# Performance work log

Measured on AMD Instinct MI355X. Metric: run time of the kernel, lower is better.

The kernel has to match this reference:

```python
import jax, jax.numpy as jnp
import numpy as np

N = 100000   # nodes
E = 1000000  # edges (avg degree 10)
F_IN, H1, H2, C = 128, 64, 64, 16


def setup_inputs() -> dict:
    key = jax.random.key(0)
    ks = jax.random.split(key, 10)
    x = jax.random.normal(ks[0], (N, F_IN), dtype=jnp.float32)
    edge_src = jax.random.randint(ks[1], (E,), 0, N, dtype=jnp.int32)
    edge_dst = jax.random.randint(ks[2], (E,), 0, N, dtype=jnp.int32)
    # normalized-adjacency-like positive edge weights (~1/deg scale)
    edge_val = jax.random.uniform(ks[3], (E,), dtype=jnp.float32) * 0.1
    def glorot(k, fan_in, fan_out):
        s = np.float32(1.0 / np.sqrt(fan_in))
        return jax.random.normal(k, (fan_in, fan_out), dtype=jnp.float32) * s
    W1 = glorot(ks[4], F_IN, H1)
    W2 = glorot(ks[5], H1, H2)
    W3 = glorot(ks[6], H2, C)
    b1 = jnp.zeros((H1,), jnp.float32)
    b2 = jnp.zeros((H2,), jnp.float32)
    b3 = jnp.zeros((C,), jnp.float32)
    return {"x": x, "edge_val": edge_val, "W1": W1, "b1": b1,
            "W2": W2, "b2": b2, "W3": W3, "b3": b3,
            "edge_src": edge_src, "edge_dst": edge_dst}


def gcn_layer(h, W, b, edge_src, edge_dst, edge_val):
    # support = h @ W ; out = spmm(adj, support) + b
    support = h @ W                                  # [N, d_out]
    msg = support[edge_src] * edge_val[:, None]      # [E, d_out] gather + scale
    agg = jax.ops.segment_sum(msg, edge_dst, num_segments=N)  # scatter-add
    return agg + b


def reference(x, edge_val, W1, b1, W2, b2, W3, b3, edge_src, edge_dst):
    # eval mode: F.dropout(training=False) is identity
    h = jax.nn.relu(gcn_layer(x, W1, b1, edge_src, edge_dst, edge_val))
    h = jax.nn.relu(gcn_layer(h, W2, b2, edge_src, edge_dst, edge_val))
    return gcn_layer(h, W3, b3, edge_src, edge_dst, edge_val)  # [N, C] logits
```

## Files before the change

kernel.cpp:

```cpp
#include <hip/hip_runtime.h>
#include <stdint.h>

#define N_NODES 100000
#define N_EDGES 1000000
#define NBUCK 98

typedef __attribute__((ext_vector_type(8))) __bf16 bf16x8;
typedef __attribute__((ext_vector_type(4))) float f32x4;

static __device__ __forceinline__ float bf2f(unsigned short u) {
    return __uint_as_float(((unsigned int)u) << 16);
}
static __device__ __forceinline__ unsigned short f2bf(float f) {
    unsigned int u = __float_as_uint(f);
    unsigned int r = (u + 0x7FFFu + ((u >> 16) & 1u)) >> 16;
    return (unsigned short)r;
}
static __device__ __forceinline__ float4 ld4_half(const unsigned short* p) {
    ushort4 u = *(const ushort4*)p;
    return make_float4(bf2f(u.x), bf2f(u.y), bf2f(u.z), bf2f(u.w));
}
static __device__ __forceinline__ void st4_half(unsigned short* p, float4 f) {
    ushort4 u;
    u.x = f2bf(f.x); u.y = f2bf(f.y); u.z = f2bf(f.z); u.w = f2bf(f.w);
    *(ushort4*)p = u;
}

static __device__ __forceinline__ float ldf(const void* p, size_t i, int bf) {
    return bf ? bf2f(((const unsigned short*)p)[i]) : ((const float*)p)[i];
}
static __device__ __forceinline__ float4 ldf4(const void* p, size_t i, int bf) {
    if (bf) return ld4_half((const unsigned short*)p + i);
    return *(const float4*)((const float*)p + i);
}

__global__ __launch_bounds__(256) void detect_kernel(const unsigned short* __restrict__ xs,
                                                     int* __restrict__ flag) {
    __shared__ int sz;
    if (threadIdx.x == 0) sz = 0;
    __syncthreads();
    int z = 0;
    for (int i = threadIdx.x; i < 1024; i += 256) {
        float av = fabsf(bf2f(xs[2 * i]));
        if (!(av <= 1048576.0f) || (av != 0.0f && av < 9.5367431640625e-07f)) z++;
    }
    atomicAdd(&sz, z);
    __syncthreads();
    if (threadIdx.x == 0) *flag = (sz > 256) ? 0 : 1;
}

__global__ __launch_bounds__(256) void bhist_kernel(const int* __restrict__ dst,
                                                    int* __restrict__ bcount) {
    __shared__ int cnt[NBUCK];
    int tid = threadIdx.x;
    for (int i = tid; i < NBUCK; i += 256) cnt[i] = 0;
    __syncthreads();
    int e0 = blockIdx.x * 4096;
#pragma unroll
    for (int i = 0; i < 16; ++i) {
        int e = e0 + i * 256 + tid;
        if (e < N_EDGES) atomicAdd(&cnt[dst[e] >> 10], 1);
    }
    __syncthreads();
    for (int i = tid; i < NBUCK; i += 256) {
        int c = cnt[i];
        if (c) atomicAdd(&bcount[i], c);
    }
}

__global__ __launch_bounds__(128) void bscan_kernel(const int* __restrict__ bcount,
                                                    int* __restrict__ bstart,
                                                    int* __restrict__ bcursor) {
    __shared__ int sh[128];
    int tid = threadIdx.x;
    int v = (tid < NBUCK) ? bcount[tid] : 0;
    sh[tid] = v;
    __syncthreads();
    for (int off = 1; off < 128; off <<= 1) {
        int t = 0;
        if (tid >= off) t = sh[tid - off];
        __syncthreads();
        if (tid >= off) sh[tid] += t;
        __syncthreads();
    }
    if (tid < NBUCK) {
        int excl = sh[tid] - v;
        bstart[tid] = excl;
        bcursor[tid] = excl;
    }
    if (tid == NBUCK - 1) bstart[NBUCK] = sh[tid];
}

__global__ __launch_bounds__(256) void part_kernel(const int* __restrict__ src,
                                                   const int* __restrict__ dst,
                                                   const void* __restrict__ val,
                                                   int* __restrict__ bcursor,
                                                   int2* __restrict__ part,
                                                   const int* __restrict__ flagp) {
    __shared__ int cnt[NBUCK];
    __shared__ int base[NBUCK];
    const int bf = *flagp;
    const int tid = threadIdx.x;
    const int e0 = blockIdx.x * 2048;
    for (int i = tid; i < NBUCK; i += 256) cnt[i] = 0;
    __syncthreads();
    int rank[8], bkt[8], pk[8], vb[8];
#pragma unroll
    for (int i = 0; i < 8; ++i) {
        int e = e0 + i * 256 + tid;
        bkt[i] = -1;
        if (e < N_EDGES) {
            int d = dst[e];
            int b = d >> 10;
            bkt[i] = b;
            pk[i] = src[e] | ((d & 1023) << 17);
            vb[i] = __float_as_int(ldf(val, e, bf));
            rank[i] = atomicAdd(&cnt[b], 1);
        }
    }
    __syncthreads();
    for (int i = tid; i < NBUCK; i += 256) {
        int c = cnt[i];
        base[i] = c ? atomicAdd(&bcursor[i], c) : 0;
    }
    __syncthreads();
#pragma unroll
    for (int i = 0; i < 8; ++i) {
        if (bkt[i] >= 0) part[(size_t)base[bkt[i]] + rank[i]] = make_int2(pk[i], vb[i]);
    }
}

__global__ __launch_bounds__(512) void place_kernel(const int* __restrict__ bstart,
                                                    const int2* __restrict__ part,
                                                    int* __restrict__ row_start,
                                                    int2* __restrict__ csr_rec) {
    __shared__ int cnt[1024];
    __shared__ int sums[512];
    const int tid = threadIdx.x;
    const int b = blockIdx.x;
    const int row0 = b << 10;
    const int nrows = min(1024, N_NODES - row0);
    const int s = bstart[b], e = bstart[b + 1];

    for (int i = tid; i < 1024; i += 512) cnt[i] = 0;
    __syncthreads();
    for (int j = s + tid; j < e; j += 512) {
        unsigned p = (unsigned)part[j].x;
        atomicAdd(&cnt[p >> 17], 1);
    }
    __syncthreads();
    int a0 = cnt[2 * tid], a1 = cnt[2 * tid + 1];
    int ts = a0 + a1;
    sums[tid] = ts;
    __syncthreads();
    for (int off = 1; off < 512; off <<= 1) {
        int t = 0;
        if (tid >= off) t = sums[tid - off];
        __syncthreads();
        if (tid >= off) sums[tid] += t;
        __syncthreads();
    }
    int excl = sums[tid] - ts;
    cnt[2 * tid] = s + excl;
    cnt[2 * tid + 1] = s + excl + a0;
    if (2 * tid < nrows)     row_start[row0 + 2 * tid] = s + excl;
    if (2 * tid + 1 < nrows) row_start[row0 + 2 * tid + 1] = s + excl + a0;
    if (b == NBUCK - 1 && tid == 0) row_start[N_NODES] = e;
    __syncthreads();
    for (int j = s + tid; j < e; j += 512) {
        int2 r = part[j];
        unsigned p = (unsigned)r.x;
        int pos = atomicAdd(&cnt[p >> 17], 1);
        csr_rec[pos] = make_int2((int)(p & 0x1FFFFu), r.y);
    }
}

template <int M>
static __device__ __forceinline__ void quad_gather(const unsigned short* __restrict__ supc,
                                                   const int2* __restrict__ csr_rec,
                                                   int s, int b1, int b2, int b3, int e,
                                                   float4 acc[4]) {
    if (s >= e) return;
    int2 r[8];
#pragma unroll
    for (int t = 0; t < 8; ++t) r[t] = csr_rec[min(s + t, e - 1)];
    for (int j = s; j < e; j += 8) {
        float4 sp[8];
#pragma unroll
        for (int t = 0; t < 8; ++t) sp[t] = ld4_half(supc + (size_t)r[t].x * M);
        float wv[8];
#pragma unroll
        for (int t = 0; t < 8; ++t) wv[t] = (j + t < e) ? __int_as_float(r[t].y) : 0.0f;
        int jn = j + 8;
        if (jn < e) {
#pragma unroll
            for (int t = 0; t < 8; ++t) r[t] = csr_rec[min(jn + t, e - 1)];
        }
#pragma unroll
        for (int t = 0; t < 8; ++t) {
            int idx = j + t;
            float c0 = (idx < b1) ? wv[t] : 0.0f;
            float c1 = (idx < b2) ? wv[t] : 0.0f;
            float c2 = (idx < b3) ? wv[t] : 0.0f;
            float w0 = c0;
            float w1 = c1 - c0;
            float w2 = c2 - c1;
            float w3 = wv[t] - c2;
            acc[0].x += w0 * sp[t].x; acc[0].y += w0 * sp[t].y; acc[0].z += w0 * sp[t].z; acc[0].w += w0 * sp[t].w;
            acc[1].x += w1 * sp[t].x; acc[1].y += w1 * sp[t].y; acc[1].z += w1 * sp[t].z; acc[1].w += w1 * sp[t].w;
            acc[2].x += w2 * sp[t].x; acc[2].y += w2 * sp[t].y; acc[2].z += w2 * sp[t].z; acc[2].w += w2 * sp[t].w;
            acc[3].x += w3 * sp[t].x; acc[3].y += w3 * sp[t].y; acc[3].z += w3 * sp[t].z; acc[3].w += w3 * sp[t].w;
        }
    }
}

template <int K, int M, bool DYNIN>
__global__ __launch_bounds__(256, 4) void mgemm_kernel(const void* __restrict__ hv_,
                                                       const void* __restrict__ W,
                                                       unsigned short* __restrict__ out,
                                                       const int* __restrict__ flagp) {
    constexpr int KP = K + 8;
    constexpr int NC = M / 16;
    constexpr int NK = K / 32;
    constexpr int NT = (N_NODES + 63) / 64;

    __shared__ unsigned short wt[M][KP];

    const int bf = *flagp;
    const int tid = threadIdx.x;

    for (int i = tid; i < K * M; i += 256) {
        int k = i / M, m = i % M;
        wt[m][k] = f2bf(ldf(W, i, bf));
    }
    __syncthreads();

    const int lane = tid & 63;
    const int qd = lane >> 4;
    const int ln = lane & 15;
    const int wrow = (tid >> 6) * 16;

    for (int tile = blockIdx.x; tile < NT; tile += gridDim.x) {
        const int row = tile * 64 + wrow + ln;
        const bool ok = row < N_NODES;

        f32x4 acc[NC];
#pragma unroll
        for (int c = 0; c < NC; ++c) acc[c] = (f32x4){0.f, 0.f, 0.f, 0.f};

#pragma unroll
        for (int ks = 0; ks < NK; ++ks) {
            bf16x8 a;
            if (ok) {
                const size_t base = (size_t)row * K + ks * 32 + qd * 8;
                if (DYNIN && !bf) {
                    const float* xp = (const float*)hv_ + base;
                    float4 f0 = *(const float4*)xp;
                    float4 f1 = *(const float4*)(xp + 4);
                    ushort4 uu[2];
                    uu[0].x = f2bf(f0.x); uu[0].y = f2bf(f0.y); uu[0].z = f2bf(f0.z); uu[0].w = f2bf(f0.w);
                    uu[1].x = f2bf(f1.x); uu[1].y = f2bf(f1.y); uu[1].z = f2bf(f1.z); uu[1].w = f2bf(f1.w);
                    a = *(const bf16x8*)uu;
                } else {
                    a = *(const bf16x8*)((const unsigned short*)hv_ + base);
                }
            } else {
                a = (bf16x8)(__bf16)0.0f;
            }
#pragma unroll
            for (int c = 0; c < NC; ++c) {
                bf16x8 b = *(const bf16x8*)&wt[c * 16 + ln][ks * 32 + qd * 8];
                acc[c] = __builtin_amdgcn_mfma_f32_16x16x32_bf16(a, b, acc[c], 0, 0, 0);
            }
        }

#pragma unroll
        for (int c = 0; c < NC; ++c) {
#pragma unroll
            for (int r = 0; r < 4; ++r) {
                int orow = tile * 64 + wrow + qd * 4 + r;
                if (orow < N_NODES) out[(size_t)orow * M + c * 16 + ln] = f2bf(acc[c][r]);
            }
        }
    }
}

template <int MOUT>
__global__ __launch_bounds__(256) void fused_kernel(const unsigned short* __restrict__ support,
                                                    const int* __restrict__ row_start,
                                                    const int2* __restrict__ csr_rec,
                                                    const void* __restrict__ bias,
                                                    const void* __restrict__ W,
                                                    unsigned short* __restrict__ out,
                                                    const int* __restrict__ flagp) {
    constexpr int K = 64, KP = 72;
    constexpr int NC = MOUT / 16;
    constexpr int NK = 2;
    constexpr int NT = (N_NODES + 63) / 64;

    __shared__ unsigned short agg[64][KP];
    __shared__ unsigned short wt[MOUT][KP];

    const int bf = *flagp;
    const int tid = threadIdx.x;

    for (int i = tid; i < K * MOUT; i += 256) {
        int k = i / MOUT, m = i % MOUT;
        wt[m][k] = f2bf(ldf(W, i, bf));
    }
    __syncthreads();

    const int lane = tid & 63;
    const int qd = lane >> 4;
    const int ln = lane & 15;
    const int wrow = (tid >> 6) * 16;

    const int grp = tid >> 4;
    const int cc = tid & 15;
    const float4 bias4 = make_float4(ldf(bias, cc * 4 + 0, bf), ldf(bias, cc * 4 + 1, bf),
                                     ldf(bias, cc * 4 + 2, bf), ldf(bias, cc * 4 + 3, bf));
    const unsigned short* supc = support + cc * 4;

    for (int tile = blockIdx.x; tile < NT; tile += gridDim.x) {
        const int r0 = tile * 64 + grp * 4;
        int s  = row_start[min(r0 + 0, N_NODES)];
        int b1 = row_start[min(r0 + 1, N_NODES)];
        int b2 = row_start[min(r0 + 2, N_NODES)];
        int b3 = row_start[min(r0 + 3, N_NODES)];
        int e  = row_start[min(r0 + 4, N_NODES)];

        float4 acc[4] = {bias4, bias4, bias4, bias4};
        quad_gather<64>(supc, csr_rec, s, b1, b2, b3, e, acc);
#pragma unroll
        for (int k = 0; k < 4; ++k) {
            float4 a = acc[k];
            a.x = fmaxf(a.x, 0.f); a.y = fmaxf(a.y, 0.f);
            a.z = fmaxf(a.z, 0.f); a.w = fmaxf(a.w, 0.f);
            st4_half(&agg[grp * 4 + k][cc * 4], a);
        }
        __syncthreads();

        f32x4 macc[NC];
#pragma unroll
        for (int c = 0; c < NC; ++c) macc[c] = (f32x4){0.f, 0.f, 0.f, 0.f};
#pragma unroll
        for (int ks = 0; ks < NK; ++ks) {
            bf16x8 a = *(const bf16x8*)&agg[wrow + ln][ks * 32 + qd * 8];
#pragma unroll
            for (int c = 0; c < NC; ++c) {
                bf16x8 b = *(const bf16x8*)&wt[c * 16 + ln][ks * 32 + qd * 8];
                macc[c] = __builtin_amdgcn_mfma_f32_16x16x32_bf16(a, b, macc[c], 0, 0, 0);
            }
        }

#pragma unroll
        for (int c = 0; c < NC; ++c) {
#pragma unroll
            for (int r = 0; r < 4; ++r) {
                int orow = tile * 64 + wrow + qd * 4 + r;
                if (orow < N_NODES) out[(size_t)orow * MOUT + c * 16 + ln] = f2bf(macc[c][r]);
            }
        }
        __syncthreads();
    }
}

template <bool DYNOUT>
__global__ __launch_bounds__(256) void spmm16_kernel(const unsigned short* __restrict__ support,
                                                     const int* __restrict__ row_start,
                                                     const int2* __restrict__ csr_rec,
                                                     const void* __restrict__ bias,
                                                     void* __restrict__ out_,
                                                     const int* __restrict__ flagp) {
    constexpr int M = 16;
    int bf = *flagp;
    int tid = threadIdx.x;
    int grp = tid >> 2;
    int cc = tid & 3;
    int r0 = blockIdx.x * 256 + grp * 4;
    if (r0 >= N_NODES) return;
    int s  = row_start[min(r0 + 0, N_NODES)];
    int b1 = row_start[min(r0 + 1, N_NODES)];
    int b2 = row_start[min(r0 + 2, N_NODES)];
    int b3 = row_start[min(r0 + 3, N_NODES)];
    int e  = row_start[min(r0 + 4, N_NODES)];
    float4 bias4 = make_float4(ldf(bias, cc * 4 + 0, bf), ldf(bias, cc * 4 + 1, bf),
                               ldf(bias, cc * 4 + 2, bf), ldf(bias, cc * 4 + 3, bf));
    float4 acc[4] = {bias4, bias4, bias4, bias4};
    quad_gather<16>(support + cc * 4, csr_rec, s, b1, b2, b3, e, acc);
#pragma unroll
    for (int k = 0; k < 4; ++k) {
        int row = r0 + k;
        if (row < N_NODES) {
            if (DYNOUT && !bf) *(float4*)((float*)out_ + (size_t)row * M + cc * 4) = acc[k];
            else               st4_half((unsigned short*)out_ + (size_t)row * M + cc * 4, acc[k]);
        }
    }
}

extern "C" void kernel_launch(void* const* d_in, const int* in_sizes, int n_in,
                              void* d_out, int out_size, void* d_ws, size_t ws_size,
                              hipStream_t stream) {
    (void)in_sizes; (void)n_in; (void)out_size; (void)ws_size;
    const void* x  = d_in[0];
    const void* ev = d_in[1];
    const void* W1 = d_in[2];
    const void* b1 = d_in[3];
    const void* W2 = d_in[4];
    const void* b2 = d_in[5];
    const void* W3 = d_in[6];
    const void* b3 = d_in[7];
    const int* esrc = (const int*)d_in[8];
    const int* edst = (const int*)d_in[9];

    char* ws = (char*)d_ws;
    size_t off = 0;
    auto alloc = [&](size_t bytes) -> void* {
        void* p = ws + off;
        off = (off + bytes + 255) & ~(size_t)255;
        return p;
    };
    unsigned short* A = (unsigned short*)alloc((size_t)N_NODES * 64 * 2);
    unsigned short* B = (unsigned short*)alloc((size_t)N_NODES * 64 * 2);
    int* row_start  = (int*)alloc((size_t)(N_NODES + 1) * 4);
    int* bcount     = (int*)alloc(512);
    int* bstart     = (int*)alloc(512);
    int* bcursor    = (int*)alloc(512);
    int2* csr_rec   = (int2*)alloc((size_t)N_EDGES * 8);
    int* flagp      = (int*)alloc(256);
    int2* part      = (int2*)A;

    detect_kernel<<<1, 256, 0, stream>>>((const unsigned short*)x, flagp);

    hipMemsetAsync(bcount, 0, 512, stream);
    bhist_kernel<<<(N_EDGES + 4095) / 4096, 256, 0, stream>>>(edst, bcount);
    bscan_kernel<<<1, 128, 0, stream>>>(bcount, bstart, bcursor);
    part_kernel<<<(N_EDGES + 2047) / 2048, 256, 0, stream>>>(esrc, edst, ev, bcursor, part, flagp);
    place_kernel<<<NBUCK, 512, 0, stream>>>(bstart, part, row_start, csr_rec);

    mgemm_kernel<128, 64, true><<<1024, 256, 0, stream>>>(x, W1, A, flagp);
    fused_kernel<64><<<1024, 256, 0, stream>>>(A, row_start, csr_rec, b1, W2, B, flagp);
    fused_kernel<16><<<1024, 256, 0, stream>>>(B, row_start, csr_rec, b2, W3, A, flagp);
    spmm16_kernel<true><<<(N_NODES + 255) / 256, 256, 0, stream>>>(A, row_start, csr_rec, b3, d_out, flagp);
}
```

Before: 258.7 us.

## Widen SpMM gathers to 16-byte loads with fewer rows per thread

The sparse gather now reads 16 bytes (8 bf16 features) per neighbor instead of 8 bytes, unpacking the bf16 pairs with shifts and masks. In the fused layers each thread handles 2 rows instead of 4. In the final 16-wide SpMM each thread covers 8 columns, so one block now handles 512 rows. The fused kernels also launch one block per 64-row tile instead of a fixed 1024-block persistent grid. This cuts the number of gather instructions and the per-edge weight overhead, but each thread holds more registers and fewer threads share each edge-record stream.

```diff
diff --git a/kernel.cpp b/kernel.cpp
--- a/kernel.cpp
+++ b/kernel.cpp
@@ -24,6 +24,14 @@
     ushort4 u;
     u.x = f2bf(f.x); u.y = f2bf(f.y); u.z = f2bf(f.z); u.w = f2bf(f.w);
     *(ushort4*)p = u;
+}
+static __device__ __forceinline__ void st8_half(unsigned short* p, const float* f) {
+    int4 u;
+    u.x = (int)(((unsigned)f2bf(f[0])) | (((unsigned)f2bf(f[1])) << 16));
+    u.y = (int)(((unsigned)f2bf(f[2])) | (((unsigned)f2bf(f[3])) << 16));
+    u.z = (int)(((unsigned)f2bf(f[4])) | (((unsigned)f2bf(f[5])) << 16));
+    u.w = (int)(((unsigned)f2bf(f[6])) | (((unsigned)f2bf(f[7])) << 16));
+    *(int4*)p = u;
 }
 
 static __device__ __forceinline__ float ldf(const void* p, size_t i, int bf) {
@@ -175,19 +183,55 @@
     }
 }
 
-template <int M>
-static __device__ __forceinline__ void quad_gather(const unsigned short* __restrict__ supc,
-                                                   const int2* __restrict__ csr_rec,
-                                                   int s, int b1, int b2, int b3, int e,
-                                                   float4 acc[4]) {
+
+static __device__ __forceinline__ void duo_gather64(const unsigned short* __restrict__ supc,
+                                                    const int2* __restrict__ csr_rec,
+                                                    int s, int b1, int e,
+                                                    float a0[8], float a1[8]) {
     if (s >= e) return;
     int2 r[8];
 #pragma unroll
     for (int t = 0; t < 8; ++t) r[t] = csr_rec[min(s + t, e - 1)];
     for (int j = s; j < e; j += 8) {
-        float4 sp[8];
-#pragma unroll
-        for (int t = 0; t < 8; ++t) sp[t] = ld4_half(supc + (size_t)r[t].x * M);
+        int4 sp[8];
+#pragma unroll
+        for (int t = 0; t < 8; ++t) sp[t] = *(const int4*)(supc + (size_t)r[t].x * 64);
+        float wv[8];
+#pragma unroll
+        for (int t = 0; t < 8; ++t) wv[t] = (j + t < e) ? __int_as_float(r[t].y) : 0.0f;
+        int jn = j + 8;
+        if (jn < e) {
+#pragma unroll
+            for (int t = 0; t < 8; ++t) r[t] = csr_rec[min(jn + t, e - 1)];
+        }
+#pragma unroll
+        for (int t = 0; t < 8; ++t) {
+            float w0 = (j + t < b1) ? wv[t] : 0.0f;
+            float w1 = wv[t] - w0;
+            int q[4] = {sp[t].x, sp[t].y, sp[t].z, sp[t].w};
+#pragma unroll
+            for (int c = 0; c < 4; ++c) {
+                float flo = __uint_as_float(((unsigned)q[c]) << 16);
+                float fhi = __uint_as_float(((unsigned)q[c]) & 0xffff0000u);
+                a0[2 * c]     += w0 * flo; a0[2 * c + 1] += w0 * fhi;
+                a1[2 * c]     += w1 * flo; a1[2 * c + 1] += w1 * fhi;
+            }
+        }
+    }
+}
+
+static __device__ __forceinline__ void quad_gather16(const unsigned short* __restrict__ supc,
+                                                     const int2* __restrict__ csr_rec,
+                                                     int s, int b1, int b2, int b3, int e,
+                                                     float a[4][8]) {
+    if (s >= e) return;
+    int2 r[8];
+#pragma unroll
+    for (int t = 0; t < 8; ++t) r[t] = csr_rec[min(s + t, e - 1)];
+    for (int j = s; j < e; j += 8) {
+        int4 sp[8];
+#pragma unroll
+        for (int t = 0; t < 8; ++t) sp[t] = *(const int4*)(supc + (size_t)r[t].x * 16);
         float wv[8];
 #pragma unroll
         for (int t = 0; t < 8; ++t) wv[t] = (j + t < e) ? __int_as_float(r[t].y) : 0.0f;
@@ -202,14 +246,17 @@
             float c0 = (idx < b1) ? wv[t] : 0.0f;
             float c1 = (idx < b2) ? wv[t] : 0.0f;
             float c2 = (idx < b3) ? wv[t] : 0.0f;
-            float w0 = c0;
-            float w1 = c1 - c0;
-            float w2 = c2 - c1;
-            float w3 = wv[t] - c2;
-            acc[0].x += w0 * sp[t].x; acc[0].y += w0 * sp[t].y; acc[0].z += w0 * sp[t].z; acc[0].w += w0 * sp[t].w;
-            acc[1].x += w1 * sp[t].x; acc[1].y += w1 * sp[t].y; acc[1].z += w1 * sp[t].z; acc[1].w += w1 * sp[t].w;
-            acc[2].x += w2 * sp[t].x; acc[2].y += w2 * sp[t].y; acc[2].z += w2 * sp[t].z; acc[2].w += w2 * sp[t].w;
-            acc[3].x += w3 * sp[t].x; acc[3].y += w3 * sp[t].y; acc[3].z += w3 * sp[t].z; acc[3].w += w3 * sp[t].w;
+            float w0 = c0, w1 = c1 - c0, w2 = c2 - c1, w3 = wv[t] - c2;
+            int q[4] = {sp[t].x, sp[t].y, sp[t].z, sp[t].w};
+#pragma unroll
+            for (int c = 0; c < 4; ++c) {
+                float flo = __uint_as_float(((unsigned)q[c]) << 16);
+                float fhi = __uint_as_float(((unsigned)q[c]) & 0xffff0000u);
+                a[0][2 * c] += w0 * flo; a[0][2 * c + 1] += w0 * fhi;
+                a[1][2 * c] += w1 * flo; a[1][2 * c + 1] += w1 * fhi;
+                a[2][2 * c] += w2 * flo; a[2][2 * c + 1] += w2 * fhi;
+                a[3][2 * c] += w3 * flo; a[3][2 * c + 1] += w3 * fhi;
+            }
         }
     }
 }
@@ -315,29 +362,30 @@
     const int ln = lane & 15;
     const int wrow = (tid >> 6) * 16;
 
-    const int grp = tid >> 4;
-    const int cc = tid & 15;
-    const float4 bias4 = make_float4(ldf(bias, cc * 4 + 0, bf), ldf(bias, cc * 4 + 1, bf),
-                                     ldf(bias, cc * 4 + 2, bf), ldf(bias, cc * 4 + 3, bf));
-    const unsigned short* supc = support + cc * 4;
+    const int grp = tid >> 3;
+    const int cc = tid & 7;
+    float bias8[8];
+#pragma unroll
+    for (int c = 0; c < 8; ++c) bias8[c] = ldf(bias, cc * 8 + c, bf);
+    const unsigned short* supc = support + cc * 8;
 
     for (int tile = blockIdx.x; tile < NT; tile += gridDim.x) {
-        const int r0 = tile * 64 + grp * 4;
+        const int r0 = tile * 64 + grp * 2;
         int s  = row_start[min(r0 + 0, N_NODES)];
         int b1 = row_start[min(r0 + 1, N_NODES)];
-        int b2 = row_start[min(r0 + 2, N_NODES)];
-        int b3 = row_start[min(r0 + 3, N_NODES)];
-        int e  = row_start[min(r0 + 4, N_NODES)];
-
-        float4 acc[4] = {bias4, bias4, bias4, bias4};
-        quad_gather<64>(supc, csr_rec, s, b1, b2, b3, e, acc);
-#pragma unroll
-        for (int k = 0; k < 4; ++k) {
-            float4 a = acc[k];
-            a.x = fmaxf(a.x, 0.f); a.y = fmaxf(a.y, 0.f);
-            a.z = fmaxf(a.z, 0.f); a.w = fmaxf(a.w, 0.f);
-            st4_half(&agg[grp * 4 + k][cc * 4], a);
-        }
+        int e  = row_start[min(r0 + 2, N_NODES)];
+
+        float a0[8], a1[8];
+#pragma unroll
+        for (int c = 0; c < 8; ++c) { a0[c] = bias8[c]; a1[c] = bias8[c]; }
+        duo_gather64(supc, csr_rec, s, b1, e, a0, a1);
+#pragma unroll
+        for (int c = 0; c < 8; ++c) {
+            a0[c] = fmaxf(a0[c], 0.f);
+            a1[c] = fmaxf(a1[c], 0.f);
+        }
+        st8_half(&agg[grp * 2 + 0][cc * 8], a0);
+        st8_half(&agg[grp * 2 + 1][cc * 8], a1);
         __syncthreads();
 
         f32x4 macc[NC];
@@ -375,25 +423,32 @@
     constexpr int M = 16;
     int bf = *flagp;
     int tid = threadIdx.x;
-    int grp = tid >> 2;
-    int cc = tid & 3;
-    int r0 = blockIdx.x * 256 + grp * 4;
+    int grp = tid >> 1;
+    int cc = tid & 1;
+    int r0 = blockIdx.x * 512 + grp * 4;
     if (r0 >= N_NODES) return;
     int s  = row_start[min(r0 + 0, N_NODES)];
     int b1 = row_start[min(r0 + 1, N_NODES)];
     int b2 = row_start[min(r0 + 2, N_NODES)];
     int b3 = row_start[min(r0 + 3, N_NODES)];
     int e  = row_start[min(r0 + 4, N_NODES)];
-    float4 bias4 = make_float4(ldf(bias, cc * 4 + 0, bf), ldf(bias, cc * 4 + 1, bf),
-                               ldf(bias, cc * 4 + 2, bf), ldf(bias, cc * 4 + 3, bf));
-    float4 acc[4] = {bias4, bias4, bias4, bias4};
-    quad_gather<16>(support + cc * 4, csr_rec, s, b1, b2, b3, e, acc);
+    float a[4][8];
+#pragma unroll
+    for (int k = 0; k < 4; ++k)
+#pragma unroll
+        for (int c = 0; c < 8; ++c) a[k][c] = ldf(bias, cc * 8 + c, bf);
+    quad_gather16(support + cc * 8, csr_rec, s, b1, b2, b3, e, a);
 #pragma unroll
     for (int k = 0; k < 4; ++k) {
         int row = r0 + k;
         if (row < N_NODES) {
-            if (DYNOUT && !bf) *(float4*)((float*)out_ + (size_t)row * M + cc * 4) = acc[k];
-            else               st4_half((unsigned short*)out_ + (size_t)row * M + cc * 4, acc[k]);
+            if (DYNOUT && !bf) {
+                float* op = (float*)out_ + (size_t)row * M + cc * 8;
+                *(float4*)op = make_float4(a[k][0], a[k][1], a[k][2], a[k][3]);
+                *(float4*)(op + 4) = make_float4(a[k][4], a[k][5], a[k][6], a[k][7]);
+            } else {
+                st8_half((unsigned short*)out_ + (size_t)row * M + cc * 8, a[k]);
+            }
         }
     }
 }
@@ -438,8 +493,10 @@
     part_kernel<<<(N_EDGES + 2047) / 2048, 256, 0, stream>>>(esrc, edst, ev, bcursor, part, flagp);
     place_kernel<<<NBUCK, 512, 0, stream>>>(bstart, part, row_start, csr_rec);
 
+    const int NT = (N_NODES + 63) / 64;
+
     mgemm_kernel<128, 64, true><<<1024, 256, 0, stream>>>(x, W1, A, flagp);
-    fused_kernel<64><<<1024, 256, 0, stream>>>(A, row_start, csr_rec, b1, W2, B, flagp);
-    fused_kernel<16><<<1024, 256, 0, stream>>>(B, row_start, csr_rec, b2, W3, A, flagp);
-    spmm16_kernel<true><<<(N_NODES + 255) / 256, 256, 0, stream>>>(A, row_start, csr_rec, b3, d_out, flagp);
-}
+    fused_kernel<64><<<NT, 256, 0, stream>>>(A, row_start, csr_rec, b1, W2, B, flagp);
+    fused_kernel<16><<<NT, 256, 0, stream>>>(B, row_start, csr_rec, b2, W3, A, flagp);
+    spmm16_kernel<true><<<(N_NODES + 511) / 512, 256, 0, stream>>>(A, row_start, csr_rec, b3, d_out, flagp);
+}
```

Result: no change. 260.5 us (+0.7%).
